# Performance work log

Hardware: AMD Instinct MI355X
Metric: run time of the kernel (lower is better)

## Reference

```python
import jax, jax.numpy as jnp
import numpy as np

THRESHOLD_FACTOR = 1.25


def setup_inputs() -> dict:
    key = jax.random.key(0)
    r_embed = jax.random.normal(key, (4, 2048, 4), dtype=jnp.float32)
    return {"r_embed": r_embed}


def reference(r_embed):
    # diff[b,s,t,i] = -r[b,s,i]*r[b,t,i] + r[b,s,i]  (einsum outer product + broadcast add)
    r_s = r_embed[:, :, None, :]          # [B,S,1,D]
    r_t = r_embed[:, None, :, :]          # [B,1,T,D]
    diff = r_s * (1.0 - r_t)              # [B,S,T,D]
    dist_sq = jnp.sum(diff * diff, axis=-1)                    # [B,S,T]
    phase_diff = jnp.arctan2(diff[..., 1], diff[..., 0])       # [B,S,T]
    forward_bias = 0.5 * (1.0 + jnp.cos(phase_diff)) * jnp.exp(-dist_sq)
    # global mean/std over (s,t); torch .std uses Bessel correction (ddof=1)
    mean_dist = jnp.mean(dist_sq, axis=(-1, -2), keepdims=True)
    std_dist = jnp.std(dist_sq, axis=(-1, -2), keepdims=True, ddof=1)
    std_dist = jnp.clip(std_dist, 1e-6, None)
    threshold = mean_dist + THRESHOLD_FACTOR * std_dist
    valid = (dist_sq <= threshold).astype(r_embed.dtype)
    attention = valid * forward_bias
    row_sums = jnp.sum(attention, axis=-1, keepdims=True)
    return attention / (row_sums + 1e-8)
```

## Files before the change

### kernel.cpp

```cpp
#include <hip/hip_runtime.h>
#include <math.h>

#define SEQ 2048
#define NB 4
#define THREADS 256
#define K1_BLOCKS 1024
#define ROWS_PER_K1 8

__device__ __forceinline__ float wave_reduce_add_f(float v) {
    #pragma unroll
    for (int o = 32; o > 0; o >>= 1) v += __shfl_down(v, o, 64);
    return v;
}
__device__ __forceinline__ double wave_reduce_add_d(double v) {
    #pragma unroll
    for (int o = 32; o > 0; o >>= 1) v += __shfl_down(v, o, 64);
    return v;
}

__global__ __launch_bounds__(THREADS) void k_stats(const float* __restrict__ r,
                                                   double* __restrict__ partials) {
    const int bid  = blockIdx.x;
    const int b    = bid >> 8;
    const int rblk = bid & 255;
    const float* rp = r + (size_t)b * SEQ * 4;
    __shared__ float4 u[SEQ];
    const int tid = threadIdx.x;

    #pragma unroll
    for (int j = 0; j < 8; ++j) {
        float4 v = ((const float4*)rp)[tid + THREADS * j];
        float4 w; w.x = 1.f - v.x; w.y = 1.f - v.y; w.z = 1.f - v.z; w.w = 1.f - v.w;
        u[tid + THREADS * j] = w;
    }
    __syncthreads();

    double sum = 0.0, sumsq = 0.0;
    for (int rr = 0; rr < ROWS_PER_K1; ++rr) {
        const int s = rblk * ROWS_PER_K1 + rr;
        const float rs0 = rp[4*s+0], rs1 = rp[4*s+1], rs2 = rp[4*s+2], rs3 = rp[4*s+3];
        #pragma unroll
        for (int j = 0; j < 8; ++j) {
            float4 w = u[tid + THREADS * j];
            float d0 = rs0 * w.x, d1 = rs1 * w.y, d2 = rs2 * w.z, d3 = rs3 * w.w;
            float s01  = d0*d0 + d1*d1;
            float dist = (s01 + d2*d2) + d3*d3;
            sum   += (double)dist;
            sumsq += (double)dist * (double)dist;
        }
    }

    sum   = wave_reduce_add_d(sum);
    sumsq = wave_reduce_add_d(sumsq);
    __shared__ double red[8];
    const int wid = tid >> 6, lane = tid & 63;
    if (lane == 0) { red[wid*2] = sum; red[wid*2+1] = sumsq; }
    __syncthreads();
    if (tid == 0) {
        partials[bid*2+0] = red[0] + red[2] + red[4] + red[6];
        partials[bid*2+1] = red[1] + red[3] + red[5] + red[7];
    }
}

__global__ __launch_bounds__(THREADS) void k_thresh(const double* __restrict__ partials,
                                                    float* __restrict__ thr) {
    const int b = blockIdx.x;
    const int tid = threadIdx.x;
    double s = partials[(b*256 + tid)*2 + 0];
    double q = partials[(b*256 + tid)*2 + 1];
    s = wave_reduce_add_d(s);
    q = wave_reduce_add_d(q);
    __shared__ double red[8];
    const int wid = tid >> 6, lane = tid & 63;
    if (lane == 0) { red[wid*2] = s; red[wid*2+1] = q; }
    __syncthreads();
    if (tid == 0) {
        double S0 = red[0] + red[2] + red[4] + red[6];
        double S1 = red[1] + red[3] + red[5] + red[7];
        const double N = (double)SEQ * (double)SEQ;
        double mean = S0 / N;
        double var  = (S1 - S0 * S0 / N) / (N - 1.0);
        if (var < 0.0) var = 0.0;
        double sd = sqrt(var);
        if (sd < 1e-6) sd = 1e-6;
        thr[b] = (float)(mean + 1.25 * sd);
    }
}

__global__ __launch_bounds__(THREADS) void k_attn(const float* __restrict__ r,
                                                  const float* __restrict__ thr,
                                                  float* __restrict__ out) {
    const int srow = blockIdx.x;
    const int b    = blockIdx.y;
    const float* rp = r + (size_t)b * SEQ * 4;
    __shared__ float4 u[SEQ];
    __shared__ float redf[4];
    const int tid = threadIdx.x;

    #pragma unroll
    for (int j = 0; j < 8; ++j) {
        float4 v = ((const float4*)rp)[tid + THREADS * j];
        float4 w; w.x = 1.f - v.x; w.y = 1.f - v.y; w.z = 1.f - v.z; w.w = 1.f - v.w;
        u[tid + THREADS * j] = w;
    }
    const float rs0 = rp[4*srow+0], rs1 = rp[4*srow+1];
    const float rs2 = rp[4*srow+2], rs3 = rp[4*srow+3];
    const float T = thr[b];
    __syncthreads();

    float att[8];
    float rowsum = 0.f;
    #pragma unroll
    for (int j = 0; j < 8; ++j) {
        float4 w = u[tid + THREADS * j];
        float d0 = rs0 * w.x, d1 = rs1 * w.y, d2 = rs2 * w.z, d3 = rs3 * w.w;
        float s01  = d0*d0 + d1*d1;
        float dist = (s01 + d2*d2) + d3*d3;
        float cosv = (s01 > 0.f) ? d0 * rsqrtf(s01) : 1.f;
        float bias = 0.5f * (1.f + cosv) * __expf(-dist);
        float a = (dist <= T) ? bias : 0.f;
        rowsum += a;
        att[j] = a;
    }

    float v = wave_reduce_add_f(rowsum);
    const int wid = tid >> 6, lane = tid & 63;
    if (lane == 0) redf[wid] = v;
    __syncthreads();
    const float denom = (redf[0] + redf[1] + redf[2] + redf[3]) + 1e-8f;
    const float inv = 1.0f / denom;

    float* attbuf = (float*)u;
    #pragma unroll
    for (int j = 0; j < 8; ++j) attbuf[tid + THREADS * j] = att[j] * inv;
    __syncthreads();

    float4* ob = (float4*)(out + ((size_t)b * SEQ + srow) * SEQ);
    const float4* ab = (const float4*)attbuf;
    ob[tid]           = ab[tid];
    ob[tid + THREADS] = ab[tid + THREADS];
}

extern "C" void kernel_launch(void* const* d_in, const int* in_sizes, int n_in,
                              void* d_out, int out_size, void* d_ws, size_t ws_size,
                              hipStream_t stream) {
    const float* r = (const float*)d_in[0];
    float* out = (float*)d_out;
    double* partials = (double*)d_ws;
    float* thr = (float*)((char*)d_ws + (size_t)K1_BLOCKS * 2 * sizeof(double));

    k_stats <<<dim3(K1_BLOCKS), THREADS, 0, stream>>>(r, partials);
    k_thresh<<<dim3(NB),        THREADS, 0, stream>>>(partials, thr);
    k_attn  <<<dim3(SEQ, NB),   THREADS, 0, stream>>>(r, thr, out);
}
```

Measured before the change: 99.87 us.

## Fuse threshold reduction into attention kernel and process rows per wavefront

Removes the separate threshold kernel: each attention block now reduces the per-batch double partials itself and computes the threshold inline. The attention kernel handles 8 rows per block, with each wavefront computing two full rows and normalizing them via an xor-shuffle broadcast instead of LDS and block barriers. The stats kernel accumulates in float per thread and converts to double only for the cross-lane reduction, avoiding double-precision FMAs in the inner loop. In exchange, every attention block redundantly reads and reduces 256 partials, per-thread float accumulation may lose precision in the threshold, and output stores become scalar strided writes rather than float4.

```diff
diff --git a/kernel.cpp b/kernel.cpp
--- a/kernel.cpp
+++ b/kernel.cpp
@@ -5,11 +5,11 @@
 #define NB 4
 #define THREADS 256
 #define K1_BLOCKS 1024
-#define ROWS_PER_K1 8
+#define ROWS_PER_BLK 8
 
-__device__ __forceinline__ float wave_reduce_add_f(float v) {
+__device__ __forceinline__ float wave_bcast_add_f(float v) {
     #pragma unroll
-    for (int o = 32; o > 0; o >>= 1) v += __shfl_down(v, o, 64);
+    for (int o = 1; o < 64; o <<= 1) v += __shfl_xor(v, o, 64);
     return v;
 }
 __device__ __forceinline__ double wave_reduce_add_d(double v) {
@@ -35,23 +35,22 @@
     }
     __syncthreads();
 
-    double sum = 0.0, sumsq = 0.0;
-    for (int rr = 0; rr < ROWS_PER_K1; ++rr) {
-        const int s = rblk * ROWS_PER_K1 + rr;
-        const float rs0 = rp[4*s+0], rs1 = rp[4*s+1], rs2 = rp[4*s+2], rs3 = rp[4*s+3];
+    float s_f = 0.f, q_f = 0.f;
+    for (int rr = 0; rr < ROWS_PER_BLK; ++rr) {
+        const int s = rblk * ROWS_PER_BLK + rr;
+        const float4 rs = ((const float4*)rp)[s];
         #pragma unroll
         for (int j = 0; j < 8; ++j) {
             float4 w = u[tid + THREADS * j];
-            float d0 = rs0 * w.x, d1 = rs1 * w.y, d2 = rs2 * w.z, d3 = rs3 * w.w;
-            float s01  = d0*d0 + d1*d1;
-            float dist = (s01 + d2*d2) + d3*d3;
-            sum   += (double)dist;
-            sumsq += (double)dist * (double)dist;
+            float d0 = rs.x * w.x, d1 = rs.y * w.y, d2 = rs.z * w.z, d3 = rs.w * w.w;
+            float dist = (d0*d0 + d1*d1) + (d2*d2 + d3*d3);
+            s_f += dist;
+            q_f += dist * dist;
         }
     }
 
-    sum   = wave_reduce_add_d(sum);
-    sumsq = wave_reduce_add_d(sumsq);
+    double sum   = wave_reduce_add_d((double)s_f);
+    double sumsq = wave_reduce_add_d((double)q_f);
     __shared__ double red[8];
     const int wid = tid >> 6, lane = tid & 63;
     if (lane == 0) { red[wid*2] = sum; red[wid*2+1] = sumsq; }
@@ -62,40 +61,15 @@
     }
 }
 
-__global__ __launch_bounds__(THREADS) void k_thresh(const double* __restrict__ partials,
-                                                    float* __restrict__ thr) {
-    const int b = blockIdx.x;
-    const int tid = threadIdx.x;
-    double s = partials[(b*256 + tid)*2 + 0];
-    double q = partials[(b*256 + tid)*2 + 1];
-    s = wave_reduce_add_d(s);
-    q = wave_reduce_add_d(q);
-    __shared__ double red[8];
-    const int wid = tid >> 6, lane = tid & 63;
-    if (lane == 0) { red[wid*2] = s; red[wid*2+1] = q; }
-    __syncthreads();
-    if (tid == 0) {
-        double S0 = red[0] + red[2] + red[4] + red[6];
-        double S1 = red[1] + red[3] + red[5] + red[7];
-        const double N = (double)SEQ * (double)SEQ;
-        double mean = S0 / N;
-        double var  = (S1 - S0 * S0 / N) / (N - 1.0);
-        if (var < 0.0) var = 0.0;
-        double sd = sqrt(var);
-        if (sd < 1e-6) sd = 1e-6;
-        thr[b] = (float)(mean + 1.25 * sd);
-    }
-}
-
 __global__ __launch_bounds__(THREADS) void k_attn(const float* __restrict__ r,
-                                                  const float* __restrict__ thr,
+                                                  const double* __restrict__ partials,
                                                   float* __restrict__ out) {
-    const int srow = blockIdx.x;
-    const int b    = blockIdx.y;
+    const int rb = blockIdx.x;
+    const int b  = blockIdx.y;
     const float* rp = r + (size_t)b * SEQ * 4;
     __shared__ float4 u[SEQ];
-    __shared__ float redf[4];
-    const int tid = threadIdx.x;
+    __shared__ double red[8];
+    const int tid = threadIdx.x, wid = tid >> 6, lane = tid & 63;
 
     #pragma unroll
     for (int j = 0; j < 8; ++j) {
@@ -103,42 +77,47 @@
         float4 w; w.x = 1.f - v.x; w.y = 1.f - v.y; w.z = 1.f - v.z; w.w = 1.f - v.w;
         u[tid + THREADS * j] = w;
     }
-    const float rs0 = rp[4*srow+0], rs1 = rp[4*srow+1];
-    const float rs2 = rp[4*srow+2], rs3 = rp[4*srow+3];
-    const float T = thr[b];
+
+    double s = partials[(b*256 + tid)*2 + 0];
+    double q = partials[(b*256 + tid)*2 + 1];
+    s = wave_reduce_add_d(s);
+    q = wave_reduce_add_d(q);
+    if (lane == 0) { red[wid*2] = s; red[wid*2+1] = q; }
     __syncthreads();
 
-    float att[8];
-    float rowsum = 0.f;
+    const double S0 = red[0] + red[2] + red[4] + red[6];
+    const double S1 = red[1] + red[3] + red[5] + red[7];
+    const double N = (double)SEQ * (double)SEQ;
+    double mean = S0 / N;
+    double var  = (S1 - S0 * S0 / N) / (N - 1.0);
+    if (var < 0.0) var = 0.0;
+    double sd = sqrt(var);
+    if (sd < 1e-6) sd = 1e-6;
+    const float T = (float)(mean + 1.25 * sd);
+
     #pragma unroll
-    for (int j = 0; j < 8; ++j) {
-        float4 w = u[tid + THREADS * j];
-        float d0 = rs0 * w.x, d1 = rs1 * w.y, d2 = rs2 * w.z, d3 = rs3 * w.w;
-        float s01  = d0*d0 + d1*d1;
-        float dist = (s01 + d2*d2) + d3*d3;
-        float cosv = (s01 > 0.f) ? d0 * rsqrtf(s01) : 1.f;
-        float bias = 0.5f * (1.f + cosv) * __expf(-dist);
-        float a = (dist <= T) ? bias : 0.f;
-        rowsum += a;
-        att[j] = a;
+    for (int rr = 0; rr < 2; ++rr) {
+        const int srow = rb * ROWS_PER_BLK + wid * 2 + rr;
+        const float4 rs = ((const float4*)rp)[srow];
+        float att[32];
+        float rowsum = 0.f;
+        #pragma unroll
+        for (int j = 0; j < 32; ++j) {
+            float4 w = u[lane + 64 * j];
+            float d0 = rs.x * w.x, d1 = rs.y * w.y, d2 = rs.z * w.z, d3 = rs.w * w.w;
+            float s01  = d0*d0 + d1*d1;
+            float dist = s01 + (d2*d2 + d3*d3);
+            float cosv = (s01 > 0.f) ? d0 * rsqrtf(s01) : 1.f;
+            float bias = 0.5f * (1.f + cosv) * __expf(-dist);
+            float a = (dist <= T) ? bias : 0.f;
+            rowsum += a;
+            att[j] = a;
+        }
+        const float inv = 1.0f / (wave_bcast_add_f(rowsum) + 1e-8f);
+        float* orow = out + ((size_t)b * SEQ + srow) * SEQ;
+        #pragma unroll
+        for (int j = 0; j < 32; ++j) orow[lane + 64 * j] = att[j] * inv;
     }
-
-    float v = wave_reduce_add_f(rowsum);
-    const int wid = tid >> 6, lane = tid & 63;
-    if (lane == 0) redf[wid] = v;
-    __syncthreads();
-    const float denom = (redf[0] + redf[1] + redf[2] + redf[3]) + 1e-8f;
-    const float inv = 1.0f / denom;
-
-    float* attbuf = (float*)u;
-    #pragma unroll
-    for (int j = 0; j < 8; ++j) attbuf[tid + THREADS * j] = att[j] * inv;
-    __syncthreads();
-
-    float4* ob = (float4*)(out + ((size_t)b * SEQ + srow) * SEQ);
-    const float4* ab = (const float4*)attbuf;
-    ob[tid]           = ab[tid];
-    ob[tid + THREADS] = ab[tid + THREADS];
 }
 
 extern "C" void kernel_launch(void* const* d_in, const int* in_sizes, int n_in,
@@ -147,9 +126,7 @@
     const float* r = (const float*)d_in[0];
     float* out = (float*)d_out;
     double* partials = (double*)d_ws;
-    float* thr = (float*)((char*)d_ws + (size_t)K1_BLOCKS * 2 * sizeof(double));
 
-    k_stats <<<dim3(K1_BLOCKS), THREADS, 0, stream>>>(r, partials);
-    k_thresh<<<dim3(NB),        THREADS, 0, stream>>>(partials, thr);
-    k_attn  <<<dim3(SEQ, NB),   THREADS, 0, stream>>>(r, thr, out);
+    k_stats<<<dim3(K1_BLOCKS),   THREADS, 0, stream>>>(r, partials);
+    k_attn <<<dim3(SEQ/ROWS_PER_BLK, NB), THREADS, 0, stream>>>(r, partials, out);
 }
```

New measurement: 97.87 us. 1.02x faster.
